# Performance work log

Hardware: AMD Instinct MI355X
Metric: run time of the kernel (lower is better)

The kernel has to match this reference:

```python
import jax, jax.numpy as jnp
import numpy as np
import math

B, S, D, H = 2, 2048, 1024, 16
DH = D // H  # head_dim = 64


def setup_inputs() -> dict:
    key = jax.random.key(0)
    k0, k1, k2 = jax.random.split(key, 3)
    x = jax.random.normal(k0, (B, S, D), dtype=jnp.float32)
    Wi = jax.random.normal(k1, (3 * D, D), dtype=jnp.float32) * 0.02  # torch (out,in) layout
    bi = jnp.zeros((3 * D,), dtype=jnp.float32)
    Wo = jax.random.normal(k2, (D, D), dtype=jnp.float32) * 0.02
    bo = jnp.zeros((D,), dtype=jnp.float32)
    return {"x": x, "Wi": Wi, "bi": bi, "Wo": Wo, "bo": bo, "causal_mask": 1}


def reference(x, Wi, bi, Wo, bo, causal_mask):
    b, s, d = x.shape
    # fused QKV projection: nn.Linear applies x @ W.T + b
    qkv = x @ Wi.T + bi                      # (b, s, 3d)
    q, k, v = jnp.split(qkv, 3, axis=-1)
    # (b, s, d) -> (b, h, s, dh)
    def to_heads(t):
        return t.reshape(b, s, H, DH).transpose(0, 2, 1, 3)
    q, k, v = to_heads(q), to_heads(k), to_heads(v)
    scores = jnp.einsum("bhqd,bhkd->bhqk", q, k)  # (b, h, s, s)
    if causal_mask:
        # mask strictly-upper triangle with -inf BEFORE scaling (as in source; -inf unaffected)
        tri = jnp.triu(jnp.ones((s, s), dtype=bool), k=1)
        scores = jnp.where(tri, -jnp.inf, scores)
    scores = scores / math.sqrt(DH)
    weight = jax.nn.softmax(scores, axis=-1)
    out = jnp.einsum("bhqk,bhkd->bhqd", weight, v)  # (b, h, s, dh)
    out = out.transpose(0, 2, 1, 3).reshape(b, s, d)
    return out @ Wo.T + bo
```

## Files before the change

kernel.cpp:

```cpp
#include <hip/hip_runtime.h>
#include <hip/hip_bf16.h>
#include <stdint.h>

#define B_    2
#define S_    2048
#define D_    1024
#define H_    16
#define DH_   64
#define MTOT  (B_*S_)
#define NQKV  (3*D_)

typedef __attribute__((ext_vector_type(8))) short  bf16x8;
typedef __attribute__((ext_vector_type(4))) short  bf16x4;
typedef __attribute__((ext_vector_type(4))) float  f32x4;
typedef __attribute__((ext_vector_type(8))) unsigned short u16x8;
typedef unsigned short ushort_t;

__device__ __forceinline__ ushort_t f2bf(float f) {
  union { float f; unsigned int i; } v; v.f = f;
  unsigned int r = v.i + 0x7FFF + ((v.i >> 16) & 1);
  return (ushort_t)(r >> 16);
}

__device__ __forceinline__ unsigned cvt_pk_bf16(float lo, float hi) {
  unsigned r;
  asm("v_cvt_pk_bf16_f32 %0, %1, %2" : "=v"(r) : "v"(lo), "v"(hi));
  return r;
}

__device__ __forceinline__ float fexp2(float x) {
  float r;
  asm("v_exp_f32 %0, %1" : "=v"(r) : "v"(x));
  return r;
}

#if __has_builtin(__builtin_amdgcn_mfma_f32_16x16x16_bf16)
__device__ __forceinline__ f32x4 mfma16(bf16x4 a, bf16x4 b, f32x4 c) {
  return __builtin_amdgcn_mfma_f32_16x16x16_bf16(a, b, c, 0, 0, 0);
}
#elif __has_builtin(__builtin_amdgcn_mfma_f32_16x16x16bf16_1k)
__device__ __forceinline__ f32x4 mfma16(bf16x4 a, bf16x4 b, f32x4 c) {
  return __builtin_amdgcn_mfma_f32_16x16x16bf16_1k(a, b, c, 0, 0, 0);
}
#else
__device__ __forceinline__ f32x4 mfma16(bf16x4 a, bf16x4 b, f32x4 c) {
  asm volatile("v_mfma_f32_16x16x16_bf16 %0, %1, %2, %0"
               : "+v"(c) : "v"(a), "v"(b));
  return c;
}
#endif

__device__ __forceinline__ void gl_lds16(const ushort_t* g, ushort_t* l) {
  __builtin_amdgcn_global_load_lds(
      (const __attribute__((address_space(1))) unsigned int*)g,
      (__attribute__((address_space(3))) unsigned int*)l, 16, 0, 0);
}

#define CVN1 (MTOT*D_/8)
#define CVN2 (NQKV*D_/8)
#define CVN3 (D_*D_/8)
__global__ __launch_bounds__(256) void cvt_all(
    const float* __restrict__ x, const float* __restrict__ Wi, const float* __restrict__ Wo,
    ushort_t* __restrict__ xb, ushort_t* __restrict__ Wib, ushort_t* __restrict__ Wob) {
  int i = blockIdx.x * blockDim.x + threadIdx.x;
  const float* src; ushort_t* dst; int k;
  if (i < CVN1)            { src = x;  dst = xb;  k = i; }
  else if (i < CVN1+CVN2)  { src = Wi; dst = Wib; k = i - CVN1; }
  else                     { src = Wo; dst = Wob; k = i - CVN1 - CVN2; }
  const float4* s4 = (const float4*)src;
  float4 a = s4[2*k], b = s4[2*k+1];
  u16x8 o;
  o[0]=f2bf(a.x); o[1]=f2bf(a.y); o[2]=f2bf(a.z); o[3]=f2bf(a.w);
  o[4]=f2bf(b.x); o[5]=f2bf(b.y); o[6]=f2bf(b.z); o[7]=f2bf(b.w);
  ((u16x8*)dst)[k] = o;
}

#define BKg 32
#define QSCALE 0.18033688011112042f
__global__ __launch_bounds__(256) void gemm_qkv(
    const ushort_t* __restrict__ Abf, const ushort_t* __restrict__ Bbf,
    const float* __restrict__ bias,
    ushort_t* __restrict__ qb, ushort_t* __restrict__ kb, ushort_t* __restrict__ vb) {
  __shared__ __align__(16) ushort_t Al[128*BKg];
  __shared__ __align__(16) ushort_t Bl[128*BKg];
  int tid = threadIdx.x;
  int w = tid >> 6, lane = tid & 63;
  int wrow = (w >> 1) * 64, wcol = (w & 1) * 64;
  int m0 = blockIdx.y * 128, n0 = blockIdx.x * 128;
  const int K = D_;
  f32x4 zero = {0.f, 0.f, 0.f, 0.f};
  f32x4 acc[4][4];
  for (int i=0;i<4;i++) for (int j=0;j<4;j++) acc[i][j] = zero;

  for (int k0 = 0; k0 < K; k0 += BKg) {
    __syncthreads();
    for (int it = 0; it < 2; ++it) {
      int c = it*256 + tid;
      int row = c >> 2, cc = c & 3;
      int lbase = (it*256 + w*64) * 8;
      gl_lds16(Abf + (size_t)(m0+row)*K + k0 + cc*8, Al + lbase);
      gl_lds16(Bbf + (size_t)(n0+row)*K + k0 + cc*8, Bl + lbase);
    }
    asm volatile("s_waitcnt vmcnt(0)" ::: "memory");
    __syncthreads();
    int kof = (lane >> 4) * 8;
    bf16x8 af[4], bfr[4];
    for (int i=0;i<4;i++) af[i]  = *(const bf16x8*)(Al + (wrow + i*16 + (lane&15))*BKg + kof);
    for (int j=0;j<4;j++) bfr[j] = *(const bf16x8*)(Bl + (wcol + j*16 + (lane&15))*BKg + kof);
    for (int i=0;i<4;i++)
      for (int j=0;j<4;j++)
        acc[i][j] = __builtin_amdgcn_mfma_f32_16x16x32_bf16(af[i], bfr[j], acc[i][j], 0, 0, 0);
  }
  for (int i=0;i<4;i++)
    for (int j=0;j<4;j++)
      for (int r=0;r<4;r++) {
        int gm = m0 + wrow + i*16 + (lane>>4)*4 + r;
        int gn = n0 + wcol + j*16 + (lane&15);
        float v = acc[i][j][r] + bias[gn];
        int b = gm >> 11, s = gm & (S_-1);
        int sect = gn >> 10, hn = gn & (D_-1);
        int hh = hn >> 6, d = hn & 63;
        size_t idx = (((size_t)(b*H_ + hh))*S_ + s)*DH_ + d;
        if (sect == 0) v *= QSCALE;
        ushort_t val = f2bf(v);
        if (sect == 0) qb[idx] = val;
        else if (sect == 1) kb[idx] = val;
        else vb[idx] = val;
      }
}

__global__ __launch_bounds__(256) void transpose_v(
    const ushort_t* __restrict__ vb, ushort_t* __restrict__ vtb) {
  __shared__ ushort_t T[64*72];
  int bh = blockIdx.y;
  int s0 = blockIdx.x * 64;
  int tid = threadIdx.x;
  const ushort_t* src = vb + (size_t)bh * S_ * DH_;
  ushort_t* dst = vtb + (size_t)bh * DH_ * S_;
  for (int it = 0; it < 2; ++it) {
    int c = it*256 + tid;
    int row = c >> 3, cc = c & 7;
    *(uint4*)&T[row*72 + cc*8] = *(const uint4*)(src + (size_t)(s0+row)*DH_ + cc*8);
  }
  __syncthreads();
  for (int it = 0; it < 2; ++it) {
    int c = it*256 + tid;
    int d = c >> 3, sc = c & 7;
    u16x8 o;
    #pragma unroll
    for (int e = 0; e < 8; ++e) o[e] = T[(sc*8+e)*72 + d];
    *(u16x8*)(dst + (size_t)d*S_ + s0 + sc*8) = o;
  }
}

#define KVB 64
#define DTHR 8.0f
__global__ __launch_bounds__(256) void attn_fwd(
    const ushort_t* __restrict__ qb, const ushort_t* __restrict__ kb,
    const ushort_t* __restrict__ vtb, ushort_t* __restrict__ attnb,
    const int* __restrict__ causal) {
  int wg = blockIdx.x;
  int xcd = wg & 7;
  int rest = wg >> 3;
  int bh = (rest & 3) * 8 + xcd;
  int pairIdx = rest >> 2;
  int b = bh >> 4, h = bh & 15;
  int tid = threadIdx.x, w = tid >> 6, lane = tid & 63;
  int g = lane >> 4, q16 = lane & 15;
  const ushort_t* qh  = qb  + (size_t)bh * S_ * DH_;
  const ushort_t* kh  = kb  + (size_t)bh * S_ * DH_;
  const ushort_t* vth = vtb + (size_t)bh * DH_ * S_;
  __shared__ __align__(16) ushort_t Kl[3][KVB*64];
  __shared__ __align__(16) ushort_t Vtl[3][64*KVB];
  bool use_causal = (causal[0] != 0);

  int p1 = pairIdx, p2 = 31 - pairIdx;
  int nkv1 = use_causal ? (p1 + 1) : (S_/KVB);
  int nkv2 = use_causal ? (p2 + 1) : (S_/KVB);
  int total = nkv1 + nkv2;
  int qw1 = p1*64 + w*16, qw2 = p2*64 + w*16;

  bf16x8 qA0 = *(const bf16x8*)(qh + (size_t)(qw1 + q16)*DH_ +  0 + g*8);
  bf16x8 qA1 = *(const bf16x8*)(qh + (size_t)(qw1 + q16)*DH_ + 32 + g*8);
  bf16x8 qB0 = *(const bf16x8*)(qh + (size_t)(qw2 + q16)*DH_ +  0 + g*8);
  bf16x8 qB1 = *(const bf16x8*)(qh + (size_t)(qw2 + q16)*DH_ + 32 + g*8);

  int c0 = tid, c1 = tid + 256;
  int r0 = c0 >> 3, sw0 = ((c0 & 7) ^ (r0 & 7)) * 8;
  int r1 = c1 >> 3, sw1 = ((c1 & 7) ^ (r1 & 7)) * 8;
  const ushort_t* kp0 = kh + r0*DH_ + sw0;
  const ushort_t* kp1 = kh + r1*DH_ + sw1;
  const ushort_t* vp0 = vth + (size_t)r0*S_ + sw0;
  const ushort_t* vp1 = vth + (size_t)r1*S_ + sw1;

  auto stage = [&](int it, int buf) {
    int t = (it < nkv1) ? it : (it - nkv1);
    size_t kadv = (size_t)(t*KVB) * DH_;
    int vadv = t*KVB;
    gl_lds16(kp0 + kadv, &Kl[buf][c0*8]);
    gl_lds16(kp1 + kadv, &Kl[buf][c1*8]);
    gl_lds16(vp0 + vadv, &Vtl[buf][c0*8]);
    gl_lds16(vp1 + vadv, &Vtl[buf][c1*8]);
  };

  f32x4 zero = {0.f,0.f,0.f,0.f};
  f32x4 o[4];
  #pragma unroll
  for (int dt=0;dt<4;dt++) o[dt] = zero;
  float mrun = -1e30f, lrun = 0.f;
  bf16x8 qc0 = qA0, qc1 = qA1;

  auto epilogue = [&](int qw) {
    float li0 = 1.f / __shfl(lrun, 4*g + 0, 64);
    float li1 = 1.f / __shfl(lrun, 4*g + 1, 64);
    float li2 = 1.f / __shfl(lrun, 4*g + 2, 64);
    float li3 = 1.f / __shfl(lrun, 4*g + 3, 64);
    #pragma unroll
    for (int r=0;r<4;r++) {
      float li = (r==0)?li0:(r==1)?li1:(r==2)?li2:li3;
      int q = qw + 4*g + r;
      #pragma unroll
      for (int dt=0;dt<4;dt++) {
        int d = dt*16 + q16;
        attnb[((size_t)(b*S_ + q))*D_ + h*DH_ + d] = f2bf(o[dt][r] * li);
      }
    }
  };

  stage(0, 0);
  stage(1, 1);
  asm volatile("s_waitcnt vmcnt(4)" ::: "memory");
  __syncthreads();

  for (int it = 0; it < total; ++it) {
    if (it == nkv1) {
      epilogue(qw1);
      #pragma unroll
      for (int dt=0;dt<4;dt++) o[dt] = zero;
      mrun = -1e30f; lrun = 0.f;
      qc0 = qB0; qc1 = qB1;
    }
    int t    = (it < nkv1) ? it : (it - nkv1);
    int nkvc = (it < nkv1) ? nkv1 : nkv2;
    int cur = it % 3;
    if (it + 2 < total) stage(it + 2, (it + 2) % 3);

    f32x4 sacc[4];
    #pragma unroll
    for (int j=0;j<4;j++) sacc[j] = zero;
    #pragma unroll
    for (int kk=0;kk<2;kk++) {
      bf16x8 qf = kk ? qc1 : qc0;
      #pragma unroll
      for (int j=0;j<4;j++) {
        int row = j*16 + q16;
        int slot = (kk*4 + g) ^ (row & 7);
        bf16x8 kf = *(const bf16x8*)(&Kl[cur][row*64 + slot*8]);
        sacc[j] = __builtin_amdgcn_mfma_f32_16x16x32_bf16(kf, qf, sacc[j], 0, 0, 0);
      }
    }
    if (use_causal && t == nkvc-1) {
      int qrel = 16*w + q16;
      #pragma unroll
      for (int j=0;j<4;j++)
        #pragma unroll
        for (int r=0;r<4;r++)
          if (16*j + 4*g + r > qrel) sacc[j][r] = -1e30f;
    }
    float m0v = fmaxf(fmaxf(sacc[0][0], sacc[0][1]), fmaxf(sacc[0][2], sacc[0][3]));
    float m1v = fmaxf(fmaxf(sacc[1][0], sacc[1][1]), fmaxf(sacc[1][2], sacc[1][3]));
    float m2v = fmaxf(fmaxf(sacc[2][0], sacc[2][1]), fmaxf(sacc[2][2], sacc[2][3]));
    float m3v = fmaxf(fmaxf(sacc[3][0], sacc[3][1]), fmaxf(sacc[3][2], sacc[3][3]));
    float mx = fmaxf(fmaxf(m0v, m1v), fmaxf(m2v, m3v));
    mx = fmaxf(mx, __shfl_xor(mx, 16, 64));
    mx = fmaxf(mx, __shfl_xor(mx, 32, 64));
    if (!__all(mx - mrun <= DTHR)) {
      float mnew = fmaxf(mrun, mx);
      float alpha = fexp2(mrun - mnew);
      lrun *= alpha;
      float av0 = __shfl(alpha, 4*g + 0, 64);
      float av1 = __shfl(alpha, 4*g + 1, 64);
      float av2 = __shfl(alpha, 4*g + 2, 64);
      float av3 = __shfl(alpha, 4*g + 3, 64);
      #pragma unroll
      for (int dt=0;dt<4;dt++) {
        o[dt][0] *= av0; o[dt][1] *= av1; o[dt][2] *= av2; o[dt][3] *= av3;
      }
      mrun = mnew;
    }
    float p[4][4];
    float rs = 0.f;
    #pragma unroll
    for (int j=0;j<4;j++)
      #pragma unroll
      for (int r=0;r<4;r++) {
        p[j][r] = fexp2(sacc[j][r] - mrun);
        rs += p[j][r];
      }
    rs += __shfl_xor(rs, 16, 64);
    rs += __shfl_xor(rs, 32, 64);
    lrun += rs;
    #pragma unroll
    for (int s=0;s<4;s++) {
      union { unsigned u[2]; bf16x4 v; } pk;
      pk.u[0] = cvt_pk_bf16(p[s][0], p[s][1]);
      pk.u[1] = cvt_pk_bf16(p[s][2], p[s][3]);
      int E = 16*s + 4*g;
      #pragma unroll
      for (int dt=0;dt<4;dt++) {
        int row = dt*16 + q16;
        int off = row*64 + ((E >> 3) ^ (row & 7))*8 + (E & 7);
        bf16x4 vf = *(const bf16x4*)(&Vtl[cur][off]);
        o[dt] = mfma16(pk.v, vf, o[dt]);
      }
    }
    if (it + 2 < total) {
      asm volatile("s_waitcnt vmcnt(4)" ::: "memory");
    } else {
      asm volatile("s_waitcnt vmcnt(0)" ::: "memory");
    }
    __syncthreads();
  }
  epilogue(qw2);
}

__global__ __launch_bounds__(256) void gemm_out(
    const ushort_t* __restrict__ Abf, const ushort_t* __restrict__ Bbf,
    const float* __restrict__ bias, float* __restrict__ out) {
  __shared__ __align__(16) ushort_t Al[128*BKg];
  __shared__ __align__(16) ushort_t Bl[128*BKg];
  int tid = threadIdx.x;
  int w = tid >> 6, lane = tid & 63;
  int wrow = (w >> 1) * 64, wcol = (w & 1) * 64;
  int m0 = blockIdx.y * 128, n0 = blockIdx.x * 128;
  const int K = D_;
  f32x4 zero = {0.f,0.f,0.f,0.f};
  f32x4 acc[4][4];
  for (int i=0;i<4;i++) for (int j=0;j<4;j++) acc[i][j] = zero;

  for (int k0 = 0; k0 < K; k0 += BKg) {
    __syncthreads();
    for (int it = 0; it < 2; ++it) {
      int c = it*256 + tid;
      int row = c >> 2, cc = c & 3;
      int lbase = (it*256 + w*64) * 8;
      gl_lds16(Abf + (size_t)(m0+row)*K + k0 + cc*8, Al + lbase);
      gl_lds16(Bbf + (size_t)(n0+row)*K + k0 + cc*8, Bl + lbase);
    }
    asm volatile("s_waitcnt vmcnt(0)" ::: "memory");
    __syncthreads();
    int kof = (lane >> 4) * 8;
    bf16x8 af[4], bfr[4];
    for (int i=0;i<4;i++) af[i]  = *(const bf16x8*)(Al + (wrow + i*16 + (lane&15))*BKg + kof);
    for (int j=0;j<4;j++) bfr[j] = *(const bf16x8*)(Bl + (wcol + j*16 + (lane&15))*BKg + kof);
    for (int i=0;i<4;i++)
      for (int j=0;j<4;j++)
        acc[i][j] = __builtin_amdgcn_mfma_f32_16x16x32_bf16(af[i], bfr[j], acc[i][j], 0, 0, 0);
  }
  for (int i=0;i<4;i++)
    for (int j=0;j<4;j++)
      for (int r=0;r<4;r++) {
        int gm = m0 + wrow + i*16 + (lane>>4)*4 + r;
        int gn = n0 + wcol + j*16 + (lane&15);
        out[(size_t)gm*D_ + gn] = acc[i][j][r] + bias[gn];
      }
}

extern "C" void kernel_launch(void* const* d_in, const int* in_sizes, int n_in,
                              void* d_out, int out_size, void* d_ws, size_t ws_size,
                              hipStream_t stream) {
  const float* x  = (const float*)d_in[0];
  const float* Wi = (const float*)d_in[1];
  const float* bi = (const float*)d_in[2];
  const float* Wo = (const float*)d_in[3];
  const float* bo = (const float*)d_in[4];
  const int* causal = (const int*)d_in[5];
  float* out = (float*)d_out;

  ushort_t* xb   = (ushort_t*)d_ws;
  ushort_t* Wib  = xb  + (size_t)MTOT*D_;
  ushort_t* Wob  = Wib + (size_t)NQKV*D_;
  ushort_t* qbuf = Wob + (size_t)D_*D_;
  ushort_t* kbuf = qbuf + (size_t)B_*H_*S_*DH_;
  ushort_t* vbuf = kbuf + (size_t)B_*H_*S_*DH_;
  ushort_t* attnb = vbuf + (size_t)B_*H_*S_*DH_;
  ushort_t* vtb  = xb;

  int ntot = CVN1 + CVN2 + CVN3;
  cvt_all<<<(ntot+255)/256, 256, 0, stream>>>(x, Wi, Wo, xb, Wib, Wob);

  gemm_qkv<<<dim3(NQKV/128, MTOT/128), 256, 0, stream>>>(xb, Wib, bi, qbuf, kbuf, vbuf);
  transpose_v<<<dim3(S_/64, B_*H_), 256, 0, stream>>>(vbuf, vtb);
  attn_fwd<<<512, 256, 0, stream>>>(qbuf, kbuf, vtb, attnb, causal);
  gemm_out<<<dim3(D_/128, MTOT/128), 256, 0, stream>>>(attnb, Wob, bo, out);
}
```

Baseline: 123.4 us.

## Use 8-wave blocks with 128-row query tiles instead of paired query blocks

The attention kernel now launches 512-thread blocks in which each of the 8 waves owns 16 query rows of a 128-row tile. Previously each 4-wave block processed two 64-row query blocks (a front/back pair) one after the other. K/V tiles are now loaded once per block and shared by 8 waves, which halves the global-to-LDS staging per thread and replaces the pair-based load balancing with largest-first scheduling (qblk reversed). The causal mask now applies per wave on diagonal tiles, and __syncthreads is replaced by a raw s_barrier. In exchange, blocks are no longer balanced against each other, and waves whose rows end early still iterate over fully masked tiles.

```diff
diff --git a/kernel.cpp b/kernel.cpp
--- a/kernel.cpp
+++ b/kernel.cpp
@@ -155,7 +155,7 @@
 
 #define KVB 64
 #define DTHR 8.0f
-__global__ __launch_bounds__(256) void attn_fwd(
+__global__ __launch_bounds__(512) void attn_fwd(
     const ushort_t* __restrict__ qb, const ushort_t* __restrict__ kb,
     const ushort_t* __restrict__ vtb, ushort_t* __restrict__ attnb,
     const int* __restrict__ causal) {
@@ -163,7 +163,7 @@
   int xcd = wg & 7;
   int rest = wg >> 3;
   int bh = (rest & 3) * 8 + xcd;
-  int pairIdx = rest >> 2;
+  int qblk = 15 - (rest >> 2);
   int b = bh >> 4, h = bh & 15;
   int tid = threadIdx.x, w = tid >> 6, lane = tid & 63;
   int g = lane >> 4, q16 = lane & 15;
@@ -174,33 +174,19 @@
   __shared__ __align__(16) ushort_t Vtl[3][64*KVB];
   bool use_causal = (causal[0] != 0);
 
-  int p1 = pairIdx, p2 = 31 - pairIdx;
-  int nkv1 = use_causal ? (p1 + 1) : (S_/KVB);
-  int nkv2 = use_causal ? (p2 + 1) : (S_/KVB);
-  int total = nkv1 + nkv2;
-  int qw1 = p1*64 + w*16, qw2 = p2*64 + w*16;
-
-  bf16x8 qA0 = *(const bf16x8*)(qh + (size_t)(qw1 + q16)*DH_ +  0 + g*8);
-  bf16x8 qA1 = *(const bf16x8*)(qh + (size_t)(qw1 + q16)*DH_ + 32 + g*8);
-  bf16x8 qB0 = *(const bf16x8*)(qh + (size_t)(qw2 + q16)*DH_ +  0 + g*8);
-  bf16x8 qB1 = *(const bf16x8*)(qh + (size_t)(qw2 + q16)*DH_ + 32 + g*8);
-
-  int c0 = tid, c1 = tid + 256;
-  int r0 = c0 >> 3, sw0 = ((c0 & 7) ^ (r0 & 7)) * 8;
-  int r1 = c1 >> 3, sw1 = ((c1 & 7) ^ (r1 & 7)) * 8;
-  const ushort_t* kp0 = kh + r0*DH_ + sw0;
-  const ushort_t* kp1 = kh + r1*DH_ + sw1;
-  const ushort_t* vp0 = vth + (size_t)r0*S_ + sw0;
-  const ushort_t* vp1 = vth + (size_t)r1*S_ + sw1;
-
-  auto stage = [&](int it, int buf) {
-    int t = (it < nkv1) ? it : (it - nkv1);
-    size_t kadv = (size_t)(t*KVB) * DH_;
-    int vadv = t*KVB;
-    gl_lds16(kp0 + kadv, &Kl[buf][c0*8]);
-    gl_lds16(kp1 + kadv, &Kl[buf][c1*8]);
-    gl_lds16(vp0 + vadv, &Vtl[buf][c0*8]);
-    gl_lds16(vp1 + vadv, &Vtl[buf][c1*8]);
+  int nkv = use_causal ? (2*qblk + 2) : (S_/KVB);
+  int qw = qblk*128 + w*16;
+
+  bf16x8 qc0 = *(const bf16x8*)(qh + (size_t)(qw + q16)*DH_ +  0 + g*8);
+  bf16x8 qc1 = *(const bf16x8*)(qh + (size_t)(qw + q16)*DH_ + 32 + g*8);
+
+  int r0 = tid >> 3, sw0 = ((tid & 7) ^ (r0 & 7)) * 8;
+  const ushort_t* kp0 = kh  + (size_t)r0 * DH_ + sw0;
+  const ushort_t* vp0 = vth + (size_t)r0 * S_  + sw0;
+
+  auto stage = [&](int t, int buf) {
+    gl_lds16(kp0 + (size_t)(t*KVB) * DH_, &Kl[buf][tid*8]);
+    gl_lds16(vp0 + t*KVB,                 &Vtl[buf][tid*8]);
   };
 
   f32x4 zero = {0.f,0.f,0.f,0.f};
@@ -208,42 +194,16 @@
   #pragma unroll
   for (int dt=0;dt<4;dt++) o[dt] = zero;
   float mrun = -1e30f, lrun = 0.f;
-  bf16x8 qc0 = qA0, qc1 = qA1;
-
-  auto epilogue = [&](int qw) {
-    float li0 = 1.f / __shfl(lrun, 4*g + 0, 64);
-    float li1 = 1.f / __shfl(lrun, 4*g + 1, 64);
-    float li2 = 1.f / __shfl(lrun, 4*g + 2, 64);
-    float li3 = 1.f / __shfl(lrun, 4*g + 3, 64);
-    #pragma unroll
-    for (int r=0;r<4;r++) {
-      float li = (r==0)?li0:(r==1)?li1:(r==2)?li2:li3;
-      int q = qw + 4*g + r;
-      #pragma unroll
-      for (int dt=0;dt<4;dt++) {
-        int d = dt*16 + q16;
-        attnb[((size_t)(b*S_ + q))*D_ + h*DH_ + d] = f2bf(o[dt][r] * li);
-      }
-    }
-  };
 
   stage(0, 0);
   stage(1, 1);
-  asm volatile("s_waitcnt vmcnt(4)" ::: "memory");
-  __syncthreads();
-
-  for (int it = 0; it < total; ++it) {
-    if (it == nkv1) {
-      epilogue(qw1);
-      #pragma unroll
-      for (int dt=0;dt<4;dt++) o[dt] = zero;
-      mrun = -1e30f; lrun = 0.f;
-      qc0 = qB0; qc1 = qB1;
-    }
-    int t    = (it < nkv1) ? it : (it - nkv1);
-    int nkvc = (it < nkv1) ? nkv1 : nkv2;
+  asm volatile("s_waitcnt vmcnt(2)" ::: "memory");
+  __builtin_amdgcn_s_barrier();
+
+  for (int it = 0; it < nkv; ++it) {
     int cur = it % 3;
-    if (it + 2 < total) stage(it + 2, (it + 2) % 3);
+    int kvbase = it * KVB;
+    if (it + 2 < nkv) stage(it + 2, (it + 2) % 3);
 
     f32x4 sacc[4];
     #pragma unroll
@@ -259,13 +219,13 @@
         sacc[j] = __builtin_amdgcn_mfma_f32_16x16x32_bf16(kf, qf, sacc[j], 0, 0, 0);
       }
     }
-    if (use_causal && t == nkvc-1) {
-      int qrel = 16*w + q16;
+    if (use_causal && kvbase + KVB - 1 > qw) {
+      int qd = qw + q16 - kvbase;
       #pragma unroll
       for (int j=0;j<4;j++)
         #pragma unroll
         for (int r=0;r<4;r++)
-          if (16*j + 4*g + r > qrel) sacc[j][r] = -1e30f;
+          if (16*j + 4*g + r > qd) sacc[j][r] = -1e30f;
     }
     float m0v = fmaxf(fmaxf(sacc[0][0], sacc[0][1]), fmaxf(sacc[0][2], sacc[0][3]));
     float m1v = fmaxf(fmaxf(sacc[1][0], sacc[1][1]), fmaxf(sacc[1][2], sacc[1][3]));
@@ -314,14 +274,27 @@
         o[dt] = mfma16(pk.v, vf, o[dt]);
       }
     }
-    if (it + 2 < total) {
-      asm volatile("s_waitcnt vmcnt(4)" ::: "memory");
+    if (it + 2 < nkv) {
+      asm volatile("s_waitcnt vmcnt(2)" ::: "memory");
     } else {
       asm volatile("s_waitcnt vmcnt(0)" ::: "memory");
     }
-    __syncthreads();
-  }
-  epilogue(qw2);
+    __builtin_amdgcn_s_barrier();
+  }
+  float li0 = 1.f / __shfl(lrun, 4*g + 0, 64);
+  float li1 = 1.f / __shfl(lrun, 4*g + 1, 64);
+  float li2 = 1.f / __shfl(lrun, 4*g + 2, 64);
+  float li3 = 1.f / __shfl(lrun, 4*g + 3, 64);
+  #pragma unroll
+  for (int r=0;r<4;r++) {
+    float li = (r==0)?li0:(r==1)?li1:(r==2)?li2:li3;
+    int q = qw + 4*g + r;
+    #pragma unroll
+    for (int dt=0;dt<4;dt++) {
+      int d = dt*16 + q16;
+      attnb[((size_t)(b*S_ + q))*D_ + h*DH_ + d] = f2bf(o[dt][r] * li);
+    }
+  }
 }
 
 __global__ __launch_bounds__(256) void gemm_out(
@@ -391,6 +364,6 @@
 
   gemm_qkv<<<dim3(NQKV/128, MTOT/128), 256, 0, stream>>>(xb, Wib, bi, qbuf, kbuf, vbuf);
   transpose_v<<<dim3(S_/64, B_*H_), 256, 0, stream>>>(vbuf, vtb);
-  attn_fwd<<<512, 256, 0, stream>>>(qbuf, kbuf, vtb, attnb, causal);
+  attn_fwd<<<512, 512, 0, stream>>>(qbuf, kbuf, vtb, attnb, causal);
   gemm_out<<<dim3(D_/128, MTOT/128), 256, 0, stream>>>(attnb, Wob, bo, out);
 }
```

Result: no change. 123.3 us (-0.1%).
